# Performance work log

Measured on AMD Instinct MI355X. Metric: run time of the kernel, lower is better.

Reference implementation:

```python
import jax, jax.numpy as jnp
import numpy as np

T, K, E, H, I = 2048, 8, 32, 1024, 768


def setup_inputs() -> dict:
    key = jax.random.key(0)
    k0, k1, k2, k3, k4, k5 = jax.random.split(key, 6)
    sh = 1.0 / np.sqrt(H).astype(np.float32)
    si = 1.0 / np.sqrt(I).astype(np.float32)
    return {
        "hidden_states": jax.random.normal(k0, (T, H), jnp.float32),
        "top_k_index": jax.random.randint(k1, (T, K), 0, E),
        "top_k_weights": jax.random.uniform(k2, (T, K), jnp.float32),
        "gate_proj": jax.random.normal(k3, (E, I, H), jnp.float32) * sh,
        "up_proj": jax.random.normal(k4, (E, I, H), jnp.float32) * sh,
        "down_proj": jax.random.normal(k5, (E, H, I), jnp.float32) * si,
    }


def reference(hidden_states, top_k_index, top_k_weights, gate_proj, up_proj, down_proj):
    # Tokens not routed to expert e get combine weight 0, so summing the
    # weighted per-expert outputs over all experts reproduces the original
    # gather -> SwiGLU MLP -> scale -> index_add_ exactly (duplicated expert
    # hits within a token's top-k sum, matching repeated index_add_).
    n_tok = hidden_states.shape[0]
    n_exp = gate_proj.shape[0]
    combine = jnp.zeros((n_tok, n_exp), hidden_states.dtype)
    combine = combine.at[jnp.arange(n_tok)[:, None], top_k_index].add(top_k_weights)

    def body(acc, xs):
        g_w, u_w, d_w, w_e = xs  # g_w,u_w: [I,H]; d_w: [H,I]; w_e: [T]
        h = jax.nn.silu(hidden_states @ g_w.T) * (hidden_states @ u_w.T)  # [T,I]
        y = h @ d_w.T  # [T,H]
        return acc + y * w_e[:, None], None

    out, _ = jax.lax.scan(
        body,
        jnp.zeros_like(hidden_states),
        (gate_proj, up_proj, down_proj, combine.T),
    )
    return out
```

## Files before the change

kernel.cpp:

```cpp
#include <hip/hip_runtime.h>

#define T_TOK 2048
#define TOPK  8
#define NEXP  32
#define HDIM  1024
#define IDIM  768
#define NPAIR (T_TOK * TOPK)
#define BM 128
#define BK 32
#define MT_MAX (NPAIR / BM + NEXP)

typedef __attribute__((ext_vector_type(8))) short short8;
typedef __attribute__((ext_vector_type(4))) float f32x4;

__device__ __forceinline__ unsigned short f2bf(float f) {
    unsigned x = __float_as_uint(f);
    unsigned r = x + 0x7fffu + ((x >> 16) & 1u);
    return (unsigned short)(r >> 16);
}
__device__ __forceinline__ float bf2f(unsigned short u) {
    return __uint_as_float(((unsigned)u) << 16);
}
__device__ __forceinline__ short8 pack8(float4 a, float4 b) {
    short8 v;
    v[0] = (short)f2bf(a.x); v[1] = (short)f2bf(a.y);
    v[2] = (short)f2bf(a.z); v[3] = (short)f2bf(a.w);
    v[4] = (short)f2bf(b.x); v[5] = (short)f2bf(b.y);
    v[6] = (short)f2bf(b.z); v[7] = (short)f2bf(b.w);
    return v;
}

__global__ void k_init(int* counts) {
    if (threadIdx.x < NEXP) counts[threadIdx.x] = 0;
}

__global__ void k_hist(const int* __restrict__ idx, int* __restrict__ counts) {
    int p = blockIdx.x * 256 + threadIdx.x;
    atomicAdd(&counts[idx[p]], 1);
}

__global__ void k_scan(const int* __restrict__ counts, int* __restrict__ offsets,
                       int* __restrict__ mtb, int* __restrict__ cursor) {
    if (threadIdx.x == 0) {
        int tot = 0, mt = 0;
        for (int e = 0; e < NEXP; ++e) {
            offsets[e] = tot; mtb[e] = mt;
            tot += counts[e];
            mt += (counts[e] + BM - 1) / BM;
        }
        offsets[NEXP] = tot; mtb[NEXP] = mt;
    }
    if (threadIdx.x < NEXP) cursor[threadIdx.x] = 0;
}

__global__ void k_scatter(const int* __restrict__ idx, int* __restrict__ cursor,
                          const int* __restrict__ offsets, int* __restrict__ pair_token,
                          int* __restrict__ pair_slot) {
    int p = blockIdx.x * 256 + threadIdx.x;
    int e = idx[p];
    int pos = atomicAdd(&cursor[e], 1);
    int slot = offsets[e] + pos;
    pair_token[slot] = p >> 3;
    pair_slot[p] = slot;
}

__device__ __forceinline__ int idx16(int m, int c) {
    return ((m >> 4) * 4 + c) * 16 + (m & 15);
}

__global__ __launch_bounds__(256, 2) void k_gateup(
    const float* __restrict__ hidden, const float* __restrict__ gate,
    const float* __restrict__ up, const int* __restrict__ pair_token,
    const int* __restrict__ offsets, const int* __restrict__ mtb,
    unsigned short* __restrict__ h_mid)
{
    __shared__ short8 sA[512], sBg[256], sBu[256];
    __shared__ int sInfo[4];
    int tid = threadIdx.x;
    if (tid == 0) {
        int mt = blockIdx.x;
        if (mt >= mtb[NEXP]) { sInfo[0] = -1; }
        else {
            int e = 0;
            while (mtb[e + 1] <= mt) e++;
            sInfo[0] = e; sInfo[1] = offsets[e];
            sInfo[2] = offsets[e + 1] - offsets[e];
            sInfo[3] = (mt - mtb[e]) * BM;
        }
    }
    __syncthreads();
    int e = sInfo[0];
    if (e < 0) return;
    int off = sInfo[1], Me = sInfo[2], mrow0 = sInfo[3];
    int n0 = blockIdx.y * 64;

    int hm = tid >> 1, half = tid & 1;
    int rowp = mrow0 + hm;
    int tok = (rowp < Me) ? pair_token[off + rowp] : 0;
    const float4* aSrc = (const float4*)(hidden + (size_t)tok * HDIM);
    int wA0 = idx16(hm, half * 2);
    int wA1 = wA0 + 16;

    int bhm = tid >> 2, q = tid & 3;
    const float4* gSrc = (const float4*)(gate + ((size_t)e * IDIM + (n0 + bhm)) * HDIM);
    const float4* uSrc = (const float4*)(up   + ((size_t)e * IDIM + (n0 + bhm)) * HDIM);
    int wB = idx16(bhm, q);

    int wave = tid >> 6, lane = tid & 63, quad = lane >> 4, l16 = lane & 15;
    int wm = (wave & 1) * 64, wn = (wave >> 1) * 32;
    int aBase = ((wm >> 4) * 4 + quad) * 16 + l16;
    int bBase = ((wn >> 4) * 4 + quad) * 16 + l16;

    f32x4 zero = {0.f, 0.f, 0.f, 0.f};
    f32x4 accg[4][2], accu[4][2];
#pragma unroll
    for (int i = 0; i < 4; ++i)
#pragma unroll
        for (int j = 0; j < 2; ++j) { accg[i][j] = zero; accu[i][j] = zero; }

    for (int k0 = 0; k0 < HDIM; k0 += BK) {
        int abase = (k0 >> 2) + (half << 2);
        float4 a0 = aSrc[abase], a1 = aSrc[abase + 1], a2 = aSrc[abase + 2], a3 = aSrc[abase + 3];
        int bbase = (k0 >> 2) + (q << 1);
        float4 g0 = gSrc[bbase], g1 = gSrc[bbase + 1];
        float4 u0 = uSrc[bbase], u1 = uSrc[bbase + 1];
        __syncthreads();
        sA[wA0] = pack8(a0, a1); sA[wA1] = pack8(a2, a3);
        sBg[wB] = pack8(g0, g1);
        sBu[wB] = pack8(u0, u1);
        __syncthreads();
        short8 af[4];
#pragma unroll
        for (int fm = 0; fm < 4; ++fm) af[fm] = sA[aBase + fm * 64];
#pragma unroll
        for (int fn = 0; fn < 2; ++fn) {
            short8 bg = sBg[bBase + fn * 64];
            short8 bu = sBu[bBase + fn * 64];
#pragma unroll
            for (int fm = 0; fm < 4; ++fm) {
                accg[fm][fn] = __builtin_amdgcn_mfma_f32_16x16x32_bf16(af[fm], bg, accg[fm][fn], 0, 0, 0);
                accu[fm][fn] = __builtin_amdgcn_mfma_f32_16x16x32_bf16(af[fm], bu, accu[fm][fn], 0, 0, 0);
            }
        }
    }

#pragma unroll
    for (int fm = 0; fm < 4; ++fm)
#pragma unroll
        for (int fn = 0; fn < 2; ++fn)
#pragma unroll
            for (int r = 0; r < 4; ++r) {
                int mloc = wm + fm * 16 + quad * 4 + r;
                int prow = mrow0 + mloc;
                if (prow < Me) {
                    int col = n0 + wn + fn * 16 + l16;
                    float g = accg[fm][fn][r], u = accu[fm][fn][r];
                    float h = g / (1.f + __expf(-g)) * u;
                    h_mid[(size_t)(off + prow) * IDIM + col] = f2bf(h);
                }
            }
}

__global__ __launch_bounds__(256, 2) void k_down(
    const unsigned short* __restrict__ h_mid, const float* __restrict__ down,
    const int* __restrict__ offsets, const int* __restrict__ mtb,
    unsigned short* __restrict__ y_pair)
{
    __shared__ short8 sA[512], sB[512];
    __shared__ int sInfo[4];
    int tid = threadIdx.x;
    if (tid == 0) {
        int mt = blockIdx.x;
        if (mt >= mtb[NEXP]) { sInfo[0] = -1; }
        else {
            int e = 0;
            while (mtb[e + 1] <= mt) e++;
            sInfo[0] = e; sInfo[1] = offsets[e];
            sInfo[2] = offsets[e + 1] - offsets[e];
            sInfo[3] = (mt - mtb[e]) * BM;
        }
    }
    __syncthreads();
    int e = sInfo[0];
    if (e < 0) return;
    int off = sInfo[1], Me = sInfo[2], mrow0 = sInfo[3];
    int n0 = blockIdx.y * 128;

    int hm = tid >> 1, half = tid & 1;
    int rowp = mrow0 + hm;
    int arow = off + ((rowp < Me) ? rowp : 0);
    const short8* aSrc = (const short8*)(h_mid + (size_t)arow * IDIM);
    const float4* bSrc = (const float4*)(down + ((size_t)e * HDIM + (n0 + hm)) * IDIM);
    int w0 = idx16(hm, half * 2);
    int w1 = w0 + 16;

    int wave = tid >> 6, lane = tid & 63, quad = lane >> 4, l16 = lane & 15;
    int wm = (wave & 1) * 64, wn = (wave >> 1) * 64;
    int aBase = ((wm >> 4) * 4 + quad) * 16 + l16;
    int bBase = ((wn >> 4) * 4 + quad) * 16 + l16;

    f32x4 zero = {0.f, 0.f, 0.f, 0.f};
    f32x4 acc[4][4];
#pragma unroll
    for (int i = 0; i < 4; ++i)
#pragma unroll
        for (int j = 0; j < 4; ++j) acc[i][j] = zero;

    for (int k0 = 0; k0 < IDIM; k0 += BK) {
        int abase = (k0 >> 3) + (half << 1);
        short8 A0 = aSrc[abase], A1 = aSrc[abase + 1];
        int bbase = (k0 >> 2) + (half << 2);
        float4 b0 = bSrc[bbase], b1 = bSrc[bbase + 1], b2 = bSrc[bbase + 2], b3 = bSrc[bbase + 3];
        __syncthreads();
        sA[w0] = A0; sA[w1] = A1;
        sB[w0] = pack8(b0, b1); sB[w1] = pack8(b2, b3);
        __syncthreads();
        short8 af[4];
#pragma unroll
        for (int fm = 0; fm < 4; ++fm) af[fm] = sA[aBase + fm * 64];
#pragma unroll
        for (int fn = 0; fn < 4; ++fn) {
            short8 bf = sB[bBase + fn * 64];
#pragma unroll
            for (int fm = 0; fm < 4; ++fm)
                acc[fm][fn] = __builtin_amdgcn_mfma_f32_16x16x32_bf16(af[fm], bf, acc[fm][fn], 0, 0, 0);
        }
    }

#pragma unroll
    for (int fm = 0; fm < 4; ++fm)
#pragma unroll
        for (int fn = 0; fn < 4; ++fn)
#pragma unroll
            for (int r = 0; r < 4; ++r) {
                int mloc = wm + fm * 16 + quad * 4 + r;
                int prow = mrow0 + mloc;
                if (prow < Me) {
                    int col = n0 + wn + fn * 16 + l16;
                    y_pair[(size_t)(off + prow) * HDIM + col] = f2bf(acc[fm][fn][r]);
                }
            }
}

__global__ void k_reduce(const unsigned short* __restrict__ y_pair,
                         const int* __restrict__ pair_slot,
                         const float* __restrict__ topw, float* __restrict__ out)
{
    int t = blockIdx.x;
    __shared__ int ss[TOPK];
    __shared__ float sw[TOPK];
    if (threadIdx.x < TOPK) {
        ss[threadIdx.x] = pair_slot[t * TOPK + threadIdx.x];
        sw[threadIdx.x] = topw[t * TOPK + threadIdx.x];
    }
    __syncthreads();
    int c = threadIdx.x * 4;
    float a0 = 0.f, a1 = 0.f, a2 = 0.f, a3 = 0.f;
    for (int k = 0; k < TOPK; ++k) {
        const unsigned short* yr = y_pair + (size_t)ss[k] * HDIM + c;
        uint2 v = *(const uint2*)yr;
        float w = sw[k];
        a0 += w * bf2f((unsigned short)(v.x & 0xffff));
        a1 += w * bf2f((unsigned short)(v.x >> 16));
        a2 += w * bf2f((unsigned short)(v.y & 0xffff));
        a3 += w * bf2f((unsigned short)(v.y >> 16));
    }
    float4 o = {a0, a1, a2, a3};
    *(float4*)(out + (size_t)t * HDIM + c) = o;
}

extern "C" void kernel_launch(void* const* d_in, const int* in_sizes, int n_in,
                              void* d_out, int out_size, void* d_ws, size_t ws_size,
                              hipStream_t stream) {
    (void)in_sizes; (void)n_in; (void)out_size; (void)ws_size;
    const float* hidden = (const float*)d_in[0];
    const int*   tki    = (const int*)d_in[1];
    const float* tkw    = (const float*)d_in[2];
    const float* gate   = (const float*)d_in[3];
    const float* up     = (const float*)d_in[4];
    const float* down   = (const float*)d_in[5];
    float* out = (float*)d_out;

    char* w = (char*)d_ws;
    unsigned short* h_mid  = (unsigned short*)w;
    unsigned short* y_pair = (unsigned short*)(w + (size_t)NPAIR * IDIM * 2);
    int* ib = (int*)(w + (size_t)NPAIR * IDIM * 2 + (size_t)NPAIR * HDIM * 2);
    int* pair_token = ib;
    int* pair_slot  = ib + NPAIR;
    int* counts     = ib + 2 * NPAIR;
    int* cursor     = counts + NEXP;
    int* offsets    = cursor + NEXP;
    int* mtb        = offsets + NEXP + 1;

    k_init<<<1, 64, 0, stream>>>(counts);
    k_hist<<<NPAIR / 256, 256, 0, stream>>>(tki, counts);
    k_scan<<<1, 64, 0, stream>>>(counts, offsets, mtb, cursor);
    k_scatter<<<NPAIR / 256, 256, 0, stream>>>(tki, cursor, offsets, pair_token, pair_slot);
    k_gateup<<<dim3(MT_MAX, IDIM / 64), 256, 0, stream>>>(hidden, gate, up, pair_token, offsets, mtb, h_mid);
    k_down<<<dim3(MT_MAX, HDIM / 128), 256, 0, stream>>>(h_mid, down, offsets, mtb, y_pair);
    k_reduce<<<T_TOK, 256, 0, stream>>>(y_pair, pair_slot, tkw, out);
}
```

Before: 580.3 us.

## Pre-convert inputs to bf16 and stage GEMM tiles via global_load_lds

Adds separate conversion kernels that cast hidden states and the gate, up and down weights to bf16 in workspace before the grouped GEMMs. The GEMM kernels then fetch bf16 tiles straight into LDS with global_load_lds, dropping per-block fp32 loads and in-register packing, and move the second barrier to the end of each k-step. The gate/up weights are read once for conversion instead of once per token tile. The price is extra full passes over the weights (about 300MB of fp32 reads plus bf16 writes), and workspace buffers are aliased, so down_bf and y_pair reuse the gate and up bf16 regions.

```diff
diff --git a/kernel.cpp b/kernel.cpp
--- a/kernel.cpp
+++ b/kernel.cpp
@@ -21,13 +21,20 @@
 __device__ __forceinline__ float bf2f(unsigned short u) {
     return __uint_as_float(((unsigned)u) << 16);
 }
-__device__ __forceinline__ short8 pack8(float4 a, float4 b) {
-    short8 v;
-    v[0] = (short)f2bf(a.x); v[1] = (short)f2bf(a.y);
-    v[2] = (short)f2bf(a.z); v[3] = (short)f2bf(a.w);
-    v[4] = (short)f2bf(b.x); v[5] = (short)f2bf(b.y);
-    v[6] = (short)f2bf(b.z); v[7] = (short)f2bf(b.w);
-    return v;
+
+__device__ __forceinline__ void gl_lds16(const unsigned short* g, void* l) {
+    __builtin_amdgcn_global_load_lds((const __attribute__((address_space(1))) void*)g,
+                                     (__attribute__((address_space(3))) void*)l, 16, 0, 0);
+}
+
+__global__ void k_conv(const float* __restrict__ src, unsigned short* __restrict__ dst, int n4) {
+    int i = blockIdx.x * 256 + threadIdx.x;
+    if (i < n4) {
+        float4 v = ((const float4*)src)[i];
+        ushort4 o;
+        o.x = f2bf(v.x); o.y = f2bf(v.y); o.z = f2bf(v.z); o.w = f2bf(v.w);
+        ((ushort4*)dst)[i] = o;
+    }
 }
 
 __global__ void k_init(int* counts) {
@@ -64,13 +71,9 @@
     pair_slot[p] = slot;
 }
 
-__device__ __forceinline__ int idx16(int m, int c) {
-    return ((m >> 4) * 4 + c) * 16 + (m & 15);
-}
-
-__global__ __launch_bounds__(256, 2) void k_gateup(
-    const float* __restrict__ hidden, const float* __restrict__ gate,
-    const float* __restrict__ up, const int* __restrict__ pair_token,
+__global__ __launch_bounds__(256) void k_gateup(
+    const unsigned short* __restrict__ hid_bf, const unsigned short* __restrict__ gate_bf,
+    const unsigned short* __restrict__ up_bf, const int* __restrict__ pair_token,
     const int* __restrict__ offsets, const int* __restrict__ mtb,
     unsigned short* __restrict__ h_mid)
 {
@@ -94,22 +97,25 @@
     int off = sInfo[1], Me = sInfo[2], mrow0 = sInfo[3];
     int n0 = blockIdx.y * 64;
 
-    int hm = tid >> 1, half = tid & 1;
-    int rowp = mrow0 + hm;
-    int tok = (rowp < Me) ? pair_token[off + rowp] : 0;
-    const float4* aSrc = (const float4*)(hidden + (size_t)tok * HDIM);
-    int wA0 = idx16(hm, half * 2);
-    int wA1 = wA0 + 16;
-
-    int bhm = tid >> 2, q = tid & 3;
-    const float4* gSrc = (const float4*)(gate + ((size_t)e * IDIM + (n0 + bhm)) * HDIM);
-    const float4* uSrc = (const float4*)(up   + ((size_t)e * IDIM + (n0 + bhm)) * HDIM);
-    int wB = idx16(bhm, q);
-
     int wave = tid >> 6, lane = tid & 63, quad = lane >> 4, l16 = lane & 15;
+
+    int m0 = wave * 32 + l16, m1 = m0 + 16;
+    int rp0 = mrow0 + m0, rp1 = mrow0 + m1;
+    int tok0 = (rp0 < Me) ? pair_token[off + rp0] : 0;
+    int tok1 = (rp1 < Me) ? pair_token[off + rp1] : 0;
+    const unsigned short* aG0 = hid_bf + (size_t)tok0 * HDIM + quad * 8;
+    const unsigned short* aG1 = hid_bf + (size_t)tok1 * HDIM + quad * 8;
+    int nB = n0 + wave * 16 + l16;
+    const unsigned short* gG = gate_bf + ((size_t)e * IDIM + nB) * HDIM + quad * 8;
+    const unsigned short* uG = up_bf   + ((size_t)e * IDIM + nB) * HDIM + quad * 8;
+    void* ldsA0 = (void*)&sA[wave * 128];
+    void* ldsA1 = (void*)&sA[wave * 128 + 64];
+    void* ldsBg = (void*)&sBg[wave * 64];
+    void* ldsBu = (void*)&sBu[wave * 64];
+
     int wm = (wave & 1) * 64, wn = (wave >> 1) * 32;
-    int aBase = ((wm >> 4) * 4 + quad) * 16 + l16;
-    int bBase = ((wn >> 4) * 4 + quad) * 16 + l16;
+    int aBase = (wm >> 4) * 64 + quad * 16 + l16;
+    int bBase = (wn >> 4) * 64 + quad * 16 + l16;
 
     f32x4 zero = {0.f, 0.f, 0.f, 0.f};
     f32x4 accg[4][2], accu[4][2];
@@ -119,15 +125,10 @@
         for (int j = 0; j < 2; ++j) { accg[i][j] = zero; accu[i][j] = zero; }
 
     for (int k0 = 0; k0 < HDIM; k0 += BK) {
-        int abase = (k0 >> 2) + (half << 2);
-        float4 a0 = aSrc[abase], a1 = aSrc[abase + 1], a2 = aSrc[abase + 2], a3 = aSrc[abase + 3];
-        int bbase = (k0 >> 2) + (q << 1);
-        float4 g0 = gSrc[bbase], g1 = gSrc[bbase + 1];
-        float4 u0 = uSrc[bbase], u1 = uSrc[bbase + 1];
-        __syncthreads();
-        sA[wA0] = pack8(a0, a1); sA[wA1] = pack8(a2, a3);
-        sBg[wB] = pack8(g0, g1);
-        sBu[wB] = pack8(u0, u1);
+        gl_lds16(aG0 + k0, ldsA0);
+        gl_lds16(aG1 + k0, ldsA1);
+        gl_lds16(gG + k0, ldsBg);
+        gl_lds16(uG + k0, ldsBu);
         __syncthreads();
         short8 af[4];
 #pragma unroll
@@ -142,6 +143,7 @@
                 accu[fm][fn] = __builtin_amdgcn_mfma_f32_16x16x32_bf16(af[fm], bu, accu[fm][fn], 0, 0, 0);
             }
         }
+        __syncthreads();
     }
 
 #pragma unroll
@@ -161,8 +163,8 @@
             }
 }
 
-__global__ __launch_bounds__(256, 2) void k_down(
-    const unsigned short* __restrict__ h_mid, const float* __restrict__ down,
+__global__ __launch_bounds__(256) void k_down(
+    const unsigned short* __restrict__ h_mid, const unsigned short* __restrict__ down_bf,
     const int* __restrict__ offsets, const int* __restrict__ mtb,
     unsigned short* __restrict__ y_pair)
 {
@@ -186,18 +188,24 @@
     int off = sInfo[1], Me = sInfo[2], mrow0 = sInfo[3];
     int n0 = blockIdx.y * 128;
 
-    int hm = tid >> 1, half = tid & 1;
-    int rowp = mrow0 + hm;
-    int arow = off + ((rowp < Me) ? rowp : 0);
-    const short8* aSrc = (const short8*)(h_mid + (size_t)arow * IDIM);
-    const float4* bSrc = (const float4*)(down + ((size_t)e * HDIM + (n0 + hm)) * IDIM);
-    int w0 = idx16(hm, half * 2);
-    int w1 = w0 + 16;
-
     int wave = tid >> 6, lane = tid & 63, quad = lane >> 4, l16 = lane & 15;
+
+    int m0 = wave * 32 + l16, m1 = m0 + 16;
+    int rp0 = mrow0 + m0; if (rp0 >= Me) rp0 = 0;
+    int rp1 = mrow0 + m1; if (rp1 >= Me) rp1 = 0;
+    const unsigned short* aG0 = h_mid + (size_t)(off + rp0) * IDIM + quad * 8;
+    const unsigned short* aG1 = h_mid + (size_t)(off + rp1) * IDIM + quad * 8;
+    int nb0 = n0 + wave * 32 + l16, nb1 = nb0 + 16;
+    const unsigned short* bG0 = down_bf + ((size_t)e * HDIM + nb0) * IDIM + quad * 8;
+    const unsigned short* bG1 = down_bf + ((size_t)e * HDIM + nb1) * IDIM + quad * 8;
+    void* ldsA0 = (void*)&sA[wave * 128];
+    void* ldsA1 = (void*)&sA[wave * 128 + 64];
+    void* ldsB0 = (void*)&sB[wave * 128];
+    void* ldsB1 = (void*)&sB[wave * 128 + 64];
+
     int wm = (wave & 1) * 64, wn = (wave >> 1) * 64;
-    int aBase = ((wm >> 4) * 4 + quad) * 16 + l16;
-    int bBase = ((wn >> 4) * 4 + quad) * 16 + l16;
+    int aBase = (wm >> 4) * 64 + quad * 16 + l16;
+    int bBase = (wn >> 4) * 64 + quad * 16 + l16;
 
     f32x4 zero = {0.f, 0.f, 0.f, 0.f};
     f32x4 acc[4][4];
@@ -207,13 +215,10 @@
         for (int j = 0; j < 4; ++j) acc[i][j] = zero;
 
     for (int k0 = 0; k0 < IDIM; k0 += BK) {
-        int abase = (k0 >> 3) + (half << 1);
-        short8 A0 = aSrc[abase], A1 = aSrc[abase + 1];
-        int bbase = (k0 >> 2) + (half << 2);
-        float4 b0 = bSrc[bbase], b1 = bSrc[bbase + 1], b2 = bSrc[bbase + 2], b3 = bSrc[bbase + 3];
-        __syncthreads();
-        sA[w0] = A0; sA[w1] = A1;
-        sB[w0] = pack8(b0, b1); sB[w1] = pack8(b2, b3);
+        gl_lds16(aG0 + k0, ldsA0);
+        gl_lds16(aG1 + k0, ldsA1);
+        gl_lds16(bG0 + k0, ldsB0);
+        gl_lds16(bG1 + k0, ldsB1);
         __syncthreads();
         short8 af[4];
 #pragma unroll
@@ -225,6 +230,7 @@
             for (int fm = 0; fm < 4; ++fm)
                 acc[fm][fn] = __builtin_amdgcn_mfma_f32_16x16x32_bf16(af[fm], bf, acc[fm][fn], 0, 0, 0);
         }
+        __syncthreads();
     }
 
 #pragma unroll
@@ -282,9 +288,13 @@
     float* out = (float*)d_out;
 
     char* w = (char*)d_ws;
-    unsigned short* h_mid  = (unsigned short*)w;
-    unsigned short* y_pair = (unsigned short*)(w + (size_t)NPAIR * IDIM * 2);
-    int* ib = (int*)(w + (size_t)NPAIR * IDIM * 2 + (size_t)NPAIR * HDIM * 2);
+    unsigned short* h_mid   = (unsigned short*)w;
+    unsigned short* hid_bf  = (unsigned short*)(w + 25165824);
+    unsigned short* gate_bf = (unsigned short*)(w + 29360128);
+    unsigned short* up_bf   = (unsigned short*)(w + 79691776);
+    unsigned short* down_bf = gate_bf;
+    unsigned short* y_pair  = up_bf;
+    int* ib = (int*)(w + 130023424);
     int* pair_token = ib;
     int* pair_slot  = ib + NPAIR;
     int* counts     = ib + 2 * NPAIR;
@@ -292,11 +302,23 @@
     int* offsets    = cursor + NEXP;
     int* mtb        = offsets + NEXP + 1;
 
+    const int W4 = NEXP * IDIM * HDIM / 4;
+    const int H4 = T_TOK * HDIM / 4;
+
     k_init<<<1, 64, 0, stream>>>(counts);
     k_hist<<<NPAIR / 256, 256, 0, stream>>>(tki, counts);
     k_scan<<<1, 64, 0, stream>>>(counts, offsets, mtb, cursor);
     k_scatter<<<NPAIR / 256, 256, 0, stream>>>(tki, cursor, offsets, pair_token, pair_slot);
-    k_gateup<<<dim3(MT_MAX, IDIM / 64), 256, 0, stream>>>(hidden, gate, up, pair_token, offsets, mtb, h_mid);
-    k_down<<<dim3(MT_MAX, HDIM / 128), 256, 0, stream>>>(h_mid, down, offsets, mtb, y_pair);
+
+    k_conv<<<(H4 + 255) / 256, 256, 0, stream>>>(hidden, hid_bf, H4);
+    k_conv<<<(W4 + 255) / 256, 256, 0, stream>>>(gate, gate_bf, W4);
+    k_conv<<<(W4 + 255) / 256, 256, 0, stream>>>(up, up_bf, W4);
+
+    k_gateup<<<dim3(MT_MAX, IDIM / 64), 256, 0, stream>>>(hid_bf, gate_bf, up_bf,
+                                                          pair_token, offsets, mtb, h_mid);
+
+    k_conv<<<(W4 + 255) / 256, 256, 0, stream>>>(down, down_bf, W4);
+
+    k_down<<<dim3(MT_MAX, HDIM / 128), 256, 0, stream>>>(h_mid, down_bf, offsets, mtb, y_pair);
     k_reduce<<<T_TOK, 256, 0, stream>>>(y_pair, pair_slot, tkw, out);
 }
```

Result: no change. 581.0 us (+0.1%).
